# Performance work log

Hardware: AMD Instinct MI355X
Metric: run time of the kernel (lower is better)

The kernel has to match this reference:

```python
import jax, jax.numpy as jnp
import numpy as np

B, T, IN, H = 64, 512, 512, 1024


def setup_inputs() -> dict:
    key = jax.random.key(0)
    k1, k2, k3, k4, k5 = jax.random.split(key, 5)
    s_ih = 1.0 / np.sqrt(H)
    return {
        "input": jax.random.normal(k1, (B, T, IN), dtype=jnp.float32),
        "W_ih": jax.random.uniform(k2, (4 * H, IN), minval=-s_ih, maxval=s_ih, dtype=jnp.float32),
        "W_hh": jax.random.uniform(k3, (4 * H, H), minval=-s_ih, maxval=s_ih, dtype=jnp.float32),
        "b_ih": jax.random.uniform(k4, (4 * H,), minval=-s_ih, maxval=s_ih, dtype=jnp.float32),
        "b_hh": jax.random.uniform(k5, (4 * H,), minval=-s_ih, maxval=s_ih, dtype=jnp.float32),
    }


def reference(input, W_ih, W_hh, b_ih, b_hh):
    # Precompute input projections for all timesteps: [B, T, 4H]
    x_proj = jnp.einsum("bti,gi->btg", input, W_ih) + (b_ih + b_hh)

    def step(carry, xp_t):
        h, c = carry  # [B, H] each
        gates = xp_t + h @ W_hh.T  # [B, 4H]
        i, f, g, o = jnp.split(gates, 4, axis=-1)  # PyTorch gate order i,f,g,o
        i = jax.nn.sigmoid(i)
        f = jax.nn.sigmoid(f)
        g = jnp.tanh(g)
        o = jax.nn.sigmoid(o)
        c_new = f * c + i * g
        h_new = o * jnp.tanh(c_new)
        return (h_new, c_new), None

    h0 = jnp.zeros((input.shape[0], W_hh.shape[1]), dtype=input.dtype)
    c0 = jnp.zeros_like(h0)
    (h_fin, _), _ = jax.lax.scan(step, (h0, c0), jnp.swapaxes(x_proj, 0, 1))
    # h (num_layers=1, B, H) permuted to (B, 1, H)
    return h_fin[:, None, :]
```

## Files before the change

### kernel.cpp

```cpp
#include <hip/hip_runtime.h>
#include <hip/hip_bf16.h>


#define Bx 64
#define Tx 512
#define INx 512
#define Hx 1024
#define NBLK 128
#define UNITS 8
#define NBUF 65

typedef __attribute__((ext_vector_type(8))) short short8;
typedef __attribute__((ext_vector_type(4))) float floatx4;

#define ASYNC_CP(gp, lp)                                                      \
  __builtin_amdgcn_global_load_lds(                                           \
      (const __attribute__((address_space(1))) void*)(gp),                    \
      (__attribute__((address_space(3))) void*)(lp), 16, 0, 0)

__device__ __forceinline__ unsigned short f2bf(float f) {
  unsigned u = __float_as_uint(f);
  u += 0x7FFFu + ((u >> 16) & 1u);
  return (unsigned short)(u >> 16);
}
__device__ __forceinline__ float sigm(float x) { return 1.0f / (1.0f + __expf(-x)); }
__device__ __forceinline__ float tanh_(float x) { return 1.0f - 2.0f / (1.0f + __expf(2.0f * x)); }

__global__ void convert_x_kernel(const float* __restrict__ in, unsigned short* __restrict__ xT) {
  int idx = blockIdx.x * 256 + threadIdx.x;
  int lin = idx * 8;
  int t = lin >> 15;
  int rem = lin & 32767;
  int b = rem >> 9;
  int k = rem & 511;
  const float* src = in + ((((b << 9) + t) << 9) + k);
  float4 lo = *(const float4*)src;
  float4 hi = *(const float4*)(src + 4);
  short8 o;
  o[0] = (short)f2bf(lo.x); o[1] = (short)f2bf(lo.y);
  o[2] = (short)f2bf(lo.z); o[3] = (short)f2bf(lo.w);
  o[4] = (short)f2bf(hi.x); o[5] = (short)f2bf(hi.y);
  o[6] = (short)f2bf(hi.z); o[7] = (short)f2bf(hi.w);
  *(short8*)(xT + lin) = o;
}

__global__ __launch_bounds__(256, 1) void lstm_persistent(
    const float* __restrict__ W_ih, const float* __restrict__ W_hh,
    const float* __restrict__ b_ih, const float* __restrict__ b_hh,
    const unsigned short* __restrict__ xT,
    unsigned short* __restrict__ hbuf,
    unsigned int* __restrict__ bar,
    float* __restrict__ out)
{
  __shared__ short hsh[Bx * Hx];
  __shared__ short wsh[32 * INx];

  const int tid = threadIdx.x;
  const int lane = tid & 63;
  const int wv = tid >> 6;
  const int quad = lane >> 4;
  const int col = lane & 15;
  const int swz = col & 7;
  const int bid = blockIdx.x;
  const int j0 = bid * UNITS;
  const int m0 = wv * 16;

  unsigned int* leaf = bar + wv * 256;

  for (int idx = tid; idx < 32 * INx; idx += 256) {
    int n = idx >> 9;
    int k = idx & (INx - 1);
    int row = ((n >> 3) * Hx) + j0 + (n & 7);
    int c = k >> 3;
    wsh[n * INx + (((c ^ (n & 7)) << 3) | (k & 7))] = f2bf(W_ih[row * INx + k]);
  }

  short8 wf[32][2];
#pragma unroll
  for (int kt = 0; kt < 32; ++kt) {
#pragma unroll
    for (int nt = 0; nt < 2; ++nt) {
      int n = nt * 16 + col;
      int row = ((n >> 3) * Hx) + j0 + (n & 7);
      const float* p = W_hh + row * Hx + kt * 32 + quad * 8;
      short8 w;
#pragma unroll
      for (int j = 0; j < 8; ++j) w[j] = (short)f2bf(p[j]);
      wf[kt][nt] = w;
    }
  }

  float bias[2][4];
#pragma unroll
  for (int p = 0; p < 2; ++p) {
    int jl = 2 * quad + p;
#pragma unroll
    for (int gt = 0; gt < 4; ++gt) {
      int row = gt * Hx + j0 + jl;
      bias[p][gt] = b_ih[row] + b_hh[row];
    }
  }

  float cst[2] = {0.0f, 0.0f};
  float hst[2] = {0.0f, 0.0f};

  short8 xa[16];
  {
    const unsigned short* xrow = xT + (m0 + col) * INx + quad * 8;
#pragma unroll
    for (int kt = 0; kt < 16; ++kt) xa[kt] = *(const short8*)(xrow + kt * 32);
  }

  __syncthreads();

  int ridx = 0;
  for (int t = 0; t < Tx; ++t) {
    floatx4 a0a = {0.f, 0.f, 0.f, 0.f}, a0b = {0.f, 0.f, 0.f, 0.f};
    floatx4 a1a = {0.f, 0.f, 0.f, 0.f}, a1b = {0.f, 0.f, 0.f, 0.f};
    {
      const short* b0base = wsh + col * INx;
      const short* b1base = wsh + (col + 16) * INx;
#pragma unroll
      for (int kt = 0; kt < 16; ++kt) {
        int off = (((kt << 2) | quad) ^ swz) << 3;
        short8 b0 = *(const short8*)(b0base + off);
        short8 b1 = *(const short8*)(b1base + off);
        if (kt & 1) {
          a0b = __builtin_amdgcn_mfma_f32_16x16x32_bf16(xa[kt], b0, a0b, 0, 0, 0);
          a1b = __builtin_amdgcn_mfma_f32_16x16x32_bf16(xa[kt], b1, a1b, 0, 0, 0);
        } else {
          a0a = __builtin_amdgcn_mfma_f32_16x16x32_bf16(xa[kt], b0, a0a, 0, 0, 0);
          a1a = __builtin_amdgcn_mfma_f32_16x16x32_bf16(xa[kt], b1, a1a, 0, 0, 0);
        }
      }
    }

    {
      unsigned target = (unsigned)t * 16u;
      for (;;) {
        unsigned v = target;
        if (lane < 8)
          v = __hip_atomic_load(&leaf[lane * 32], __ATOMIC_RELAXED,
                                __HIP_MEMORY_SCOPE_AGENT);
        if (__all(v >= target)) break;
        __builtin_amdgcn_s_sleep(1);
      }
    }
    asm volatile("" ::: "memory");

    if ((t & 31) == 0 && t) {
      __builtin_amdgcn_fence(__ATOMIC_ACQUIRE, "agent");
    }

    int widx = ridx + 1; if (widx == NBUF) widx = 0;
    const unsigned short* hin = hbuf + (size_t)ridx * (Bx * Hx);
    unsigned short* hout = hbuf + (size_t)widx * (Bx * Hx);
    ridx = widx;
#pragma unroll
    for (int r = 0; r < 16; ++r) {
      const unsigned short* g = hin + (m0 + r) * Hx + ((lane ^ (r & 7)) << 3);
      short* l = hsh + (m0 + r) * Hx;
      ASYNC_CP(g, l);
      ASYNC_CP(g + 512, l + 512);
    }

    {
      int tn = (t + 1) & (Tx - 1);
      const unsigned short* xrow =
          xT + (size_t)tn * (Bx * INx) + (m0 + col) * INx + quad * 8;
#pragma unroll
      for (int kt = 0; kt < 16; ++kt) xa[kt] = *(const short8*)(xrow + kt * 32);
    }

    asm volatile("s_waitcnt vmcnt(0)" ::: "memory");

    const short* ab = hsh + (m0 + col) * Hx;
#pragma unroll
    for (int kt = 0; kt < 32; ++kt) {
      short8 af = *(const short8*)(ab + ((((kt << 2) | quad) ^ swz) << 3));
      if (kt & 1) {
        a0b = __builtin_amdgcn_mfma_f32_16x16x32_bf16(af, wf[kt][0], a0b, 0, 0, 0);
        a1b = __builtin_amdgcn_mfma_f32_16x16x32_bf16(af, wf[kt][1], a1b, 0, 0, 0);
      } else {
        a0a = __builtin_amdgcn_mfma_f32_16x16x32_bf16(af, wf[kt][0], a0a, 0, 0, 0);
        a1a = __builtin_amdgcn_mfma_f32_16x16x32_bf16(af, wf[kt][1], a1a, 0, 0, 0);
      }
    }
    floatx4 acc0 = a0a + a0b;
    floatx4 acc1 = a1a + a1b;

    float* gp = (float*)(hsh + wv * 16 * Hx);
#pragma unroll
    for (int i = 0; i < 4; ++i) {
      gp[(quad * 4 + i) * 33 + col] = acc0[i];
      gp[(quad * 4 + i) * 33 + 16 + col] = acc1[i];
    }

    unsigned int hpack = 0;
#pragma unroll
    for (int p = 0; p < 2; ++p) {
      int jl = 2 * quad + p;
      float gi = gp[col * 33 + jl] + bias[p][0];
      float gf = gp[col * 33 + 8 + jl] + bias[p][1];
      float gg = gp[col * 33 + 16 + jl] + bias[p][2];
      float go = gp[col * 33 + 24 + jl] + bias[p][3];
      float iv = sigm(gi);
      float fv = sigm(gf);
      float gv = tanh_(gg);
      float ov = sigm(go);
      float c = fv * cst[p] + iv * gv;
      cst[p] = c;
      float h = ov * tanh_(c);
      hst[p] = h;
      hpack |= ((unsigned int)f2bf(h)) << (16 * p);
    }
    __hip_atomic_store(
        (unsigned int*)(hout + (m0 + col) * Hx + j0 + 2 * quad), hpack,
        __ATOMIC_RELAXED, __HIP_MEMORY_SCOPE_AGENT);

    asm volatile("s_waitcnt vmcnt(0) lgkmcnt(0)" ::: "memory");
    if (lane == 0) {
      __hip_atomic_fetch_add(&leaf[(bid & 7) * 32], 1u, __ATOMIC_RELAXED,
                             __HIP_MEMORY_SCOPE_AGENT);
    }
  }

#pragma unroll
  for (int p = 0; p < 2; ++p) {
    int jl = 2 * quad + p;
    out[(m0 + col) * Hx + j0 + jl] = hst[p];
  }
}

extern "C" void kernel_launch(void* const* d_in, const int* in_sizes, int n_in,
                              void* d_out, int out_size, void* d_ws, size_t ws_size,
                              hipStream_t stream) {
  const float* input = (const float*)d_in[0];
  const float* W_ih  = (const float*)d_in[1];
  const float* W_hh  = (const float*)d_in[2];
  const float* b_ih  = (const float*)d_in[3];
  const float* b_hh  = (const float*)d_in[4];
  float* out = (float*)d_out;

  char* ws = (char*)d_ws;
  unsigned int* bar = (unsigned int*)ws;
  unsigned short* hbuf = (unsigned short*)(ws + 8192);
  unsigned short* xT = (unsigned short*)(ws + (9u << 20));

  hipMemsetAsync(ws, 0, 8192 + Bx * Hx * sizeof(unsigned short), stream);

  convert_x_kernel<<<(Bx * Tx * INx) / (256 * 8), 256, 0, stream>>>(input, xT);

  lstm_persistent<<<NBLK, 256, 0, stream>>>(W_ih, W_hh, b_ih, b_hh, xT, hbuf, bar, out);
}
```

Baseline: 2.832 ms.

## Add per-XCD barrier broadcast flags and split h staging wait into halves

Rework the per-step grid barrier so only blocks 0-15 poll the global counters. Once they see completion, they publish the step number to a per-XCD, per-wave flag that the other blocks on that XCD poll, with a periodic fallback to the counters. The next-step x prefetch moves ahead of the barrier, and the h copy into LDS is issued in two halves so the first half's MFMAs can start before the second half arrives. The aim is to cut contention on the shared barrier counters and hide copy latency, at the cost of more complex synchronisation that relies on the XCC_ID hardware register and on L2-local visibility.

```diff
diff --git a/kernel.cpp b/kernel.cpp
--- a/kernel.cpp
+++ b/kernel.cpp
@@ -50,6 +50,7 @@
     const unsigned short* __restrict__ xT,
     unsigned short* __restrict__ hbuf,
     unsigned int* __restrict__ bar,
+    unsigned int* __restrict__ xflag,
     float* __restrict__ out)
 {
   __shared__ short hsh[Bx * Hx];
@@ -66,6 +67,10 @@
   const int m0 = wv * 16;
 
   unsigned int* leaf = bar + wv * 256;
+
+  unsigned xcd;
+  asm("s_getreg_b32 %0, hwreg(HW_REG_XCC_ID, 0, 4)" : "=s"(xcd));
+  unsigned int* xf = xflag + (xcd * 4u + (unsigned)wv) * 32u;
 
   for (int idx = tid; idx < 32 * INx; idx += 256) {
     int n = idx >> 9;
@@ -136,14 +141,50 @@
     }
 
     {
-      unsigned target = (unsigned)t * 16u;
-      for (;;) {
-        unsigned v = target;
-        if (lane < 8)
-          v = __hip_atomic_load(&leaf[lane * 32], __ATOMIC_RELAXED,
-                                __HIP_MEMORY_SCOPE_AGENT);
-        if (__all(v >= target)) break;
-        __builtin_amdgcn_s_sleep(1);
+      int tn = (t + 1) & (Tx - 1);
+      const unsigned short* xrow =
+          xT + (size_t)tn * (Bx * INx) + (m0 + col) * INx + quad * 8;
+#pragma unroll
+      for (int kt = 0; kt < 16; ++kt) xa[kt] = *(const short8*)(xrow + kt * 32);
+    }
+
+    {
+      unsigned tl = (unsigned)t * 16u;
+      unsigned ts = (unsigned)t;
+      if (bid < 16) {
+        for (;;) {
+          unsigned v = tl;
+          if (lane < 8)
+            v = __hip_atomic_load(&leaf[lane * 32], __ATOMIC_RELAXED,
+                                  __HIP_MEMORY_SCOPE_AGENT);
+          if (__all(v >= tl)) break;
+          __builtin_amdgcn_s_sleep(1);
+        }
+        if (lane == 0) {
+          asm volatile("global_store_dword %0, %1, off"
+                       :: "v"(xf), "v"(ts) : "memory");
+        }
+      } else {
+        int it = 0;
+        for (;;) {
+          unsigned e;
+          asm volatile("global_load_dword %0, %1, off sc0\n\ts_waitcnt vmcnt(0)"
+                       : "=v"(e) : "v"(xf) : "memory");
+          if (e >= ts) break;
+          if ((++it & 15) == 0) {
+            unsigned v = tl;
+            if (lane < 8)
+              v = __hip_atomic_load(&leaf[lane * 32], __ATOMIC_RELAXED,
+                                    __HIP_MEMORY_SCOPE_AGENT);
+            if (__all(v >= tl)) {
+              if (lane == 0) {
+                asm volatile("global_store_dword %0, %1, off"
+                             :: "v"(xf), "v"(ts) : "memory");
+              }
+              break;
+            }
+          }
+        }
       }
     }
     asm volatile("" ::: "memory");
@@ -158,25 +199,34 @@
     ridx = widx;
 #pragma unroll
     for (int r = 0; r < 16; ++r) {
-      const unsigned short* g = hin + (m0 + r) * Hx + ((lane ^ (r & 7)) << 3);
-      short* l = hsh + (m0 + r) * Hx;
-      ASYNC_CP(g, l);
-      ASYNC_CP(g + 512, l + 512);
-    }
-
-    {
-      int tn = (t + 1) & (Tx - 1);
-      const unsigned short* xrow =
-          xT + (size_t)tn * (Bx * INx) + (m0 + col) * INx + quad * 8;
-#pragma unroll
-      for (int kt = 0; kt < 16; ++kt) xa[kt] = *(const short8*)(xrow + kt * 32);
+      ASYNC_CP(hin + (m0 + r) * Hx + ((lane ^ (r & 7)) << 3),
+               hsh + (m0 + r) * Hx);
+    }
+#pragma unroll
+    for (int r = 0; r < 16; ++r) {
+      ASYNC_CP(hin + (m0 + r) * Hx + 512 + ((lane ^ (r & 7)) << 3),
+               hsh + (m0 + r) * Hx + 512);
+    }
+
+    asm volatile("s_waitcnt vmcnt(16)" ::: "memory");
+
+    const short* ab = hsh + (m0 + col) * Hx;
+#pragma unroll
+    for (int kt = 0; kt < 16; ++kt) {
+      short8 af = *(const short8*)(ab + ((((kt << 2) | quad) ^ swz) << 3));
+      if (kt & 1) {
+        a0b = __builtin_amdgcn_mfma_f32_16x16x32_bf16(af, wf[kt][0], a0b, 0, 0, 0);
+        a1b = __builtin_amdgcn_mfma_f32_16x16x32_bf16(af, wf[kt][1], a1b, 0, 0, 0);
+      } else {
+        a0a = __builtin_amdgcn_mfma_f32_16x16x32_bf16(af, wf[kt][0], a0a, 0, 0, 0);
+        a1a = __builtin_amdgcn_mfma_f32_16x16x32_bf16(af, wf[kt][1], a1a, 0, 0, 0);
+      }
     }
 
     asm volatile("s_waitcnt vmcnt(0)" ::: "memory");
 
-    const short* ab = hsh + (m0 + col) * Hx;
-#pragma unroll
-    for (int kt = 0; kt < 32; ++kt) {
+#pragma unroll
+    for (int kt = 16; kt < 32; ++kt) {
       short8 af = *(const short8*)(ab + ((((kt << 2) | quad) ^ swz) << 3));
       if (kt & 1) {
         a0b = __builtin_amdgcn_mfma_f32_16x16x32_bf16(af, wf[kt][0], a0b, 0, 0, 0);
@@ -244,6 +294,7 @@
 
   char* ws = (char*)d_ws;
   unsigned int* bar = (unsigned int*)ws;
+  unsigned int* xflag = (unsigned int*)(ws + 4096);
   unsigned short* hbuf = (unsigned short*)(ws + 8192);
   unsigned short* xT = (unsigned short*)(ws + (9u << 20));
 
@@ -251,5 +302,6 @@
 
   convert_x_kernel<<<(Bx * Tx * INx) / (256 * 8), 256, 0, stream>>>(input, xT);
 
-  lstm_persistent<<<NBLK, 256, 0, stream>>>(W_ih, W_hh, b_ih, b_hh, xT, hbuf, bar, out);
+  lstm_persistent<<<NBLK, 256, 0, stream>>>(W_ih, W_hh, b_ih, b_hh, xT, hbuf, bar,
+                                            xflag, out);
 }
```

Result: slower. 4.721 ms (+66.7%).
